# Kernel tuning notes

Measured on AMD Instinct MI355X. Metric: run time of the kernel, lower is better.

Reference implementation:

```python
import jax, jax.numpy as jnp
import numpy as np

M_CH = 2        # channels == sources
K = 8           # NMF bases
N_ITER = 8
SWITCH_ITER = 5
ALPHA = 0.1
BETA = 0.0
EPS = 1e-10
I_BINS = 1025   # freq bins (n_fft=2048)
J_FRAMES = 4096 # STFT frames


def setup_inputs() -> dict:
    key = jax.random.key(0)
    ks = jax.random.split(key, 5)
    X = jax.random.normal(ks[0], (M_CH, J_FRAMES, I_BINS, 2), jnp.float32)
    T_s = jax.random.uniform(ks[1], (I_BINS, K), jnp.float32) * 0.1 + EPS
    V_s = jax.random.uniform(ks[2], (K, J_FRAMES), jnp.float32) * 0.1 + EPS
    T_n = jax.random.uniform(ks[3], (I_BINS, K), jnp.float32) * 0.1 + EPS
    V_n = jax.random.uniform(ks[4], (K, J_FRAMES), jnp.float32) * 0.1 + EPS
    return {"X": X, "T_s": T_s, "V_s": V_s, "T_n": T_n, "V_n": V_n}


def _ilrma_noisy(X, T_s, V_s, T_n, V_n):
    M, J, I, _ = X.shape
    eps, alpha, beta = EPS, ALPHA, BETA
    # (M,J,I,2) -> complex (I,M,J)
    Xc = (X[..., 0] + 1j * X[..., 1]).astype(jnp.complex64).transpose(2, 0, 1)
    eyeM = jnp.eye(M, dtype=jnp.complex64)
    W = jnp.broadcast_to(eyeM, (I, M, M))
    Y = jnp.einsum('inm,inj->imj', W.conj(), Xc)  # W^H X
    lam_n = jnp.ones((I,), jnp.float32)
    r_s = jnp.maximum(T_s @ V_s, eps)
    r_n = jnp.maximum(T_n @ V_n, eps)

    for it in range(N_ITER):
        if it < SWITCH_ITER:
            r_s = jnp.maximum(T_s @ V_s, eps)
            r_n = jnp.maximum(T_n @ V_n, eps)
        lam = lam_n[:, None]
        Lam = jnp.maximum(r_s + r_n * lam, eps)
        Y1 = Y[:, 0, :]
        p1 = jnp.abs(Y1) ** 2                          # (I,J)
        pn = jnp.sum(jnp.abs(Y[:, 1:, :]) ** 2, axis=1)  # (I,J)
        invL = 1.0 / Lam
        invL2 = invL * invL
        if it < SWITCH_ITER:
            # --- T_s ---
            T_s = jnp.maximum(T_s * jnp.sqrt(((p1 * invL2) @ V_s.T) / ((invL @ V_s.T) + eps)), eps)
            r_s = jnp.maximum(T_s @ V_s, eps)
            Lam = jnp.maximum(r_s + r_n * lam, eps); invL = 1.0 / Lam; invL2 = invL * invL
            # --- V_s ---
            V_s = jnp.maximum(V_s * jnp.sqrt((T_s.T @ (p1 * invL2)) / ((T_s.T @ invL) + eps)), eps)
            r_s = jnp.maximum(T_s @ V_s, eps)
            Lam = jnp.maximum(r_s + r_n * lam, eps); invL = 1.0 / Lam; invL2 = invL * invL
            inv_rn = 1.0 / r_n; inv_rn2 = inv_rn * inv_rn
            # --- T_n ---
            Tn_num = (lam * p1 * invL2) @ V_n.T + (pn * inv_rn2) @ V_n.T
            Tn_den = (lam * invL) @ V_n.T + (M - 1) * (inv_rn @ V_n.T) + eps
            T_n = jnp.maximum(T_n * jnp.sqrt(Tn_num / Tn_den), eps)
            r_n = jnp.maximum(T_n @ V_n, eps)
            Lam = jnp.maximum(r_s + r_n * lam, eps); invL = 1.0 / Lam; invL2 = invL * invL
            inv_rn = 1.0 / r_n; inv_rn2 = inv_rn * inv_rn
            # --- V_n ---
            Vn_num = T_n.T @ (lam * p1 * invL2) + T_n.T @ (pn * inv_rn2)
            Vn_den = T_n.T @ (lam * invL) + (M - 1) * (T_n.T @ inv_rn) + eps
            V_n = jnp.maximum(V_n * jnp.sqrt(Vn_num / Vn_den), eps)
            r_n = jnp.maximum(T_n @ V_n, eps)
            r_s = jnp.maximum(T_s @ V_s, eps)
            Lam = jnp.maximum(r_s + r_n * lam, eps); invL = 1.0 / Lam; invL2 = invL * invL
            # --- lambda_n ---
            lam_num = jnp.sum(r_n * p1 * invL2, axis=1)
            lam_den = jnp.sum(r_n * invL, axis=1) + eps
            lam_n = jnp.maximum(lam_n * jnp.sqrt(lam_num / lam_den), eps)
            Lam = jnp.maximum(r_s + r_n * lam_n[:, None], eps)
            # --- GEVD demixing update per frequency bin ---
            Xw_s = Xc * jnp.sqrt(1.0 / Lam)[:, None, :]
            Xw_n = Xc * jnp.sqrt(1.0 / r_n)[:, None, :]
            G_s = jnp.einsum('imj,inj->imn', Xw_s, Xw_s.conj()) / J + eps * eyeM
            G_n = jnp.einsum('imj,inj->imn', Xw_n, Xw_n.conj()) / J + eps * eyeM
            L = jnp.linalg.cholesky(G_s)
            Linv = jnp.linalg.inv(L)
            LinvH = jnp.conj(jnp.swapaxes(Linv, 1, 2))
            C = Linv @ G_n @ LinvH
            evals, evecs = jnp.linalg.eigh(C)  # ascending eigenvalues
            Vg = LinvH @ evecs                 # (I,M,M) generalized eigenvectors
            cols = []
            for m in range(M):
                h = Vg[:, :, m]                # (I,M); eigh already sorts ascending
                G = G_s if m == 0 else G_n
                quad = jnp.real(jnp.einsum('im,imn,in->i', h.conj(), G, h))
                cols.append(h / jnp.sqrt(jnp.maximum(quad, eps))[:, None])
            W = jnp.stack(cols, axis=2)
            Y = jnp.einsum('inm,inj->imj', W.conj(), Xc)
        else:
            # Phase 2: fix W, unconstrained r updates with inverse-gamma prior
            inv_rs = 1.0 / (r_s + eps); inv_rs2 = inv_rs * inv_rs
            inv_rn = 1.0 / (r_n + eps); inv_rn2 = inv_rn * inv_rn
            r_s = jnp.maximum(r_s * jnp.sqrt((p1 * invL2 + beta * inv_rs2) / (invL + (alpha + 1.0) * inv_rs + eps)), eps)
            Lam = jnp.maximum(r_s + r_n * lam, eps); invL = 1.0 / Lam; invL2 = invL * invL
            r_n = jnp.maximum(r_n * jnp.sqrt((lam * p1 * invL2 + pn * inv_rn2) / (lam * invL + (M - 1) * inv_rn + eps)), eps)
            Lam = jnp.maximum(r_s + r_n * lam, eps); invL = 1.0 / Lam; invL2 = invL * invL
            lam_num = jnp.sum(r_n * p1 * invL2, axis=1)
            lam_den = jnp.sum(r_n * invL, axis=1) + eps
            lam_n = jnp.maximum(lam_n * jnp.sqrt(lam_num / lam_den), eps)

    # Final single-channel Wiener extraction of the target, replicated over M
    Lam = jnp.maximum(r_s + r_n * lam_n[:, None], eps)
    S = (r_s / Lam) * Y[:, 0, :]                       # (I,J) complex
    S_ri = jnp.stack([jnp.real(S).T, jnp.imag(S).T], axis=-1)  # (J,I,2)
    return jnp.broadcast_to(S_ri[None], (M, J, I, 2)).astype(jnp.float32)


def reference(X, T_s, V_s, T_n, V_n):
    return _ilrma_noisy(X, T_s, V_s, T_n, V_n)
```

## Files before the change

### kernel.cpp

```cpp
#include <hip/hip_runtime.h>
#include <math.h>

#define IB 1025
#define JF 4096
#define EPSF 1e-10f
#define NCH 128

__device__ __forceinline__ void load8(const float* __restrict__ base, int i, float v[8]) {
  const float4* b4 = (const float4*)(base + i * 8);
  float4 a = b4[0], b = b4[1];
  v[0]=a.x; v[1]=a.y; v[2]=a.z; v[3]=a.w; v[4]=b.x; v[5]=b.y; v[6]=b.z; v[7]=b.w;
}
__device__ __forceinline__ float dot8(const float a[8], const float b[8]) {
  float s = a[0]*b[0];
#pragma unroll
  for (int k=1;k<8;k++) s += a[k]*b[k];
  return s;
}
__device__ __forceinline__ float dot8s(const float a[8], const float* __restrict__ b) {
  float s = a[0]*b[0];
#pragma unroll
  for (int k=1;k<8;k++) s += a[k]*b[k];
  return s;
}

#define STAGE_V32(vsh, vnh, Vs, Vn, j0) do {                                \
    int t_ = threadIdx.x;                                                   \
    int jj_ = t_ >> 3, k_ = t_ & 7;                                         \
    vsh[jj_][k_] = Vs[k_*JF + (j0) + jj_];                                  \
    vnh[jj_][k_] = Vn[k_*JF + (j0) + jj_];                                  \
    __syncthreads();                                                        \
  } while (0)

__global__ __launch_bounds__(256) void k_init(
    const float* __restrict__ Ts_in, const float* __restrict__ Vs_in,
    const float* __restrict__ Tn_in, const float* __restrict__ Vn_in,
    float* __restrict__ Ts, float* __restrict__ Vs,
    float* __restrict__ Tn, float* __restrict__ Vn,
    float* __restrict__ lam, float* __restrict__ Wm) {
  int idx = blockIdx.x * 256 + threadIdx.x;
  if (idx < 8 * JF) { Vs[idx] = Vs_in[idx]; Vn[idx] = Vn_in[idx]; }
  if (idx < IB * 8) { Ts[idx] = Ts_in[idx]; Tn[idx] = Tn_in[idx]; }
  if (idx < IB) {
    lam[idx] = 1.0f;
    float* w = Wm + idx * 8;
    w[0]=1.f; w[1]=0.f; w[2]=0.f; w[3]=0.f; w[4]=0.f; w[5]=0.f; w[6]=1.f; w[7]=0.f;
  }
}

__global__ __launch_bounds__(256) void k_p1pn_ts(const float2* __restrict__ X2,
    const float* __restrict__ Wm,
    const float* __restrict__ Ts, const float* __restrict__ Vs,
    const float* __restrict__ Tn, const float* __restrict__ Vn,
    const float* __restrict__ lam,
    float* __restrict__ p1, float* __restrict__ pn, float* __restrict__ P) {
  __shared__ float vsh[32][8], vnh[32][8];
  int tx = threadIdx.x;
  int i = blockIdx.x * 256 + tx;
  int jc = blockIdx.y;
  int j0 = jc * 32;
  STAGE_V32(vsh, vnh, Vs, Vn, j0);
  if (i >= IB) return;
  float ts[8], tn[8];
  load8(Ts, i, ts); load8(Tn, i, tn);
  float lamv = lam[i];
  const float4* W4 = (const float4*)Wm;
  float4 wa = W4[i*2], wb = W4[i*2+1];
  float num[8] = {0,0,0,0,0,0,0,0}, den[8] = {0,0,0,0,0,0,0,0};
#pragma unroll 4
  for (int jj = 0; jj < 32; jj++) {
    int j = j0 + jj;
    float2 x0 = X2[j*IB + i];
    float2 x1 = X2[(JF + j)*IB + i];
    float y0r = wa.x*x0.x + wa.y*x0.y + wa.z*x1.x + wa.w*x1.y;
    float y0i = wa.x*x0.y - wa.y*x0.x + wa.z*x1.y - wa.w*x1.x;
    float y1r = wb.x*x0.x + wb.y*x0.y + wb.z*x1.x + wb.w*x1.y;
    float y1i = wb.x*x0.y - wb.y*x0.x + wb.z*x1.y - wb.w*x1.x;
    float pv  = y0r*y0r + y0i*y0i;
    float pnv = y1r*y1r + y1i*y1i;
    p1[j*IB + i] = pv;
    pn[j*IB + i] = pnv;
    float rs = fmaxf(dot8s(ts, vsh[jj]), EPSF);
    float rn = fmaxf(dot8s(tn, vnh[jj]), EPSF);
    float iL = 1.f / fmaxf(rs + rn*lamv, EPSF);
    float a2 = pv*iL*iL;
#pragma unroll
    for (int k=0;k<8;k++){ num[k] += a2*vsh[jj][k]; den[k] += iL*vsh[jj][k]; }
  }
#pragma unroll
  for (int k=0;k<8;k++){
    P[(jc*16+k)*IB + i] = num[k];
    P[(jc*16+8+k)*IB + i] = den[k];
  }
}

__global__ __launch_bounds__(512) void k_t_final(const float* __restrict__ P, float* __restrict__ T) {
  int tx = threadIdx.x;
  int ii = tx & 63, g = tx >> 6;
  int i = blockIdx.x * 64 + ii;
  int k = blockIdx.y;
  float num = 0.f, den = 0.f;
  if (i < IB) {
    for (int t = 0; t < NCH/8; t++) {
      int c = g*(NCH/8) + t;
      num += P[(c*16+k)*IB + i];
      den += P[(c*16+8+k)*IB + i];
    }
  }
  __shared__ float red[2][8][64];
  red[0][g][ii] = num; red[1][g][ii] = den;
  __syncthreads();
  if (g == 0 && i < IB) {
    float n_ = 0.f, d_ = 0.f;
#pragma unroll
    for (int q=0;q<8;q++){ n_ += red[0][q][ii]; d_ += red[1][q][ii]; }
    float t = T[i*8+k];
    T[i*8+k] = fmaxf(t * sqrtf(n_/(d_+EPSF)), EPSF);
  }
}

__global__ __launch_bounds__(256) void k_vs(const float* __restrict__ p1,
    const float* __restrict__ Ts, float* __restrict__ Vs,
    const float* __restrict__ Tn, const float* __restrict__ Vn,
    const float* __restrict__ lam) {
  int j = blockIdx.x;
  int tx = threadIdx.x;
  float vs[8], vn[8];
#pragma unroll
  for (int k=0;k<8;k++){ vs[k]=Vs[k*JF+j]; vn[k]=Vn[k*JF+j]; }
  float acc[16];
#pragma unroll
  for (int v=0;v<16;v++) acc[v] = 0.f;
  for (int s = 0; s < 5; s++) {
    int i = s*256 + tx;
    if (i < IB) {
      float ts[8], tn[8];
      load8(Ts, i, ts); load8(Tn, i, tn);
      float lamv = lam[i];
      float pv = p1[j*IB + i];
      float rs = fmaxf(dot8(ts, vs), EPSF);
      float rn = fmaxf(dot8(tn, vn), EPSF);
      float iL = 1.f / fmaxf(rs + rn*lamv, EPSF);
      float a2 = pv*iL*iL;
#pragma unroll
      for (int k=0;k<8;k++){ acc[k] += ts[k]*a2; acc[8+k] += ts[k]*iL; }
    }
  }
  __shared__ float red[4][16];
  int wid = tx >> 6, lane = tx & 63;
#pragma unroll
  for (int v=0;v<16;v++){
    float x = acc[v];
    x += __shfl_down(x, 32, 64); x += __shfl_down(x, 16, 64);
    x += __shfl_down(x, 8, 64);  x += __shfl_down(x, 4, 64);
    x += __shfl_down(x, 2, 64);  x += __shfl_down(x, 1, 64);
    if (lane == 0) red[wid][v] = x;
  }
  __syncthreads();
  if (tx == 0) {
#pragma unroll
    for (int k=0;k<8;k++){
      float n_ = red[0][k]+red[1][k]+red[2][k]+red[3][k];
      float d_ = red[0][8+k]+red[1][8+k]+red[2][8+k]+red[3][8+k];
      Vs[k*JF+j] = fmaxf(vs[k] * sqrtf(n_/(d_+EPSF)), EPSF);
    }
  }
}

__global__ __launch_bounds__(256) void k_tn_partial(const float* __restrict__ p1,
    const float* __restrict__ pn,
    const float* __restrict__ Ts, const float* __restrict__ Vs,
    const float* __restrict__ Tn, const float* __restrict__ Vn,
    const float* __restrict__ lam, float* __restrict__ P) {
  __shared__ float vsh[32][8], vnh[32][8];
  int tx = threadIdx.x;
  int i = blockIdx.x * 256 + tx;
  int jc = blockIdx.y;
  int j0 = jc * 32;
  STAGE_V32(vsh, vnh, Vs, Vn, j0);
  if (i >= IB) return;
  float ts[8], tn[8];
  load8(Ts, i, ts); load8(Tn, i, tn);
  float lamv = lam[i];
  float num[8] = {0,0,0,0,0,0,0,0}, den[8] = {0,0,0,0,0,0,0,0};
#pragma unroll 4
  for (int jj = 0; jj < 32; jj++) {
    int j = j0 + jj;
    float pv = p1[j*IB + i];
    float pnv = pn[j*IB + i];
    float rs = fmaxf(dot8s(ts, vsh[jj]), EPSF);
    float rn = fmaxf(dot8s(tn, vnh[jj]), EPSF);
    float iL = 1.f / fmaxf(rs + rn*lamv, EPSF);
    float irn = 1.f / rn;
    float a2 = lamv*pv*iL*iL + pnv*irn*irn;
    float b2 = lamv*iL + irn;
#pragma unroll
    for (int k=0;k<8;k++){ num[k] += a2*vnh[jj][k]; den[k] += b2*vnh[jj][k]; }
  }
#pragma unroll
  for (int k=0;k<8;k++){
    P[(jc*16+k)*IB + i] = num[k];
    P[(jc*16+8+k)*IB + i] = den[k];
  }
}

__global__ __launch_bounds__(256) void k_vn(const float* __restrict__ p1,
    const float* __restrict__ pn,
    const float* __restrict__ Ts, const float* __restrict__ Vs,
    const float* __restrict__ Tn, float* __restrict__ Vn,
    const float* __restrict__ lam) {
  int j = blockIdx.x;
  int tx = threadIdx.x;
  float vs[8], vn[8];
#pragma unroll
  for (int k=0;k<8;k++){ vs[k]=Vs[k*JF+j]; vn[k]=Vn[k*JF+j]; }
  float acc[16];
#pragma unroll
  for (int v=0;v<16;v++) acc[v] = 0.f;
  for (int s = 0; s < 5; s++) {
    int i = s*256 + tx;
    if (i < IB) {
      float ts[8], tn[8];
      load8(Ts, i, ts); load8(Tn, i, tn);
      float lamv = lam[i];
      float pv = p1[j*IB + i];
      float pnv = pn[j*IB + i];
      float rs = fmaxf(dot8(ts, vs), EPSF);
      float rn = fmaxf(dot8(tn, vn), EPSF);
      float iL = 1.f / fmaxf(rs + rn*lamv, EPSF);
      float irn = 1.f / rn;
      float a2 = lamv*pv*iL*iL + pnv*irn*irn;
      float b2 = lamv*iL + irn;
#pragma unroll
      for (int k=0;k<8;k++){ acc[k] += tn[k]*a2; acc[8+k] += tn[k]*b2; }
    }
  }
  __shared__ float red[4][16];
  int wid = tx >> 6, lane = tx & 63;
#pragma unroll
  for (int v=0;v<16;v++){
    float x = acc[v];
    x += __shfl_down(x, 32, 64); x += __shfl_down(x, 16, 64);
    x += __shfl_down(x, 8, 64);  x += __shfl_down(x, 4, 64);
    x += __shfl_down(x, 2, 64);  x += __shfl_down(x, 1, 64);
    if (lane == 0) red[wid][v] = x;
  }
  __syncthreads();
  if (tx == 0) {
#pragma unroll
    for (int k=0;k<8;k++){
      float n_ = red[0][k]+red[1][k]+red[2][k]+red[3][k];
      float d_ = red[0][8+k]+red[1][8+k]+red[2][8+k]+red[3][8+k];
      Vn[k*JF+j] = fmaxf(vn[k] * sqrtf(n_/(d_+EPSF)), EPSF);
    }
  }
}

__global__ __launch_bounds__(256) void k_lam_partial(const float* __restrict__ p1,
    const float* __restrict__ Ts, const float* __restrict__ Vs,
    const float* __restrict__ Tn, const float* __restrict__ Vn,
    const float* __restrict__ lam, float* __restrict__ P) {
  __shared__ float vsh[32][8], vnh[32][8];
  int tx = threadIdx.x;
  int i = blockIdx.x * 256 + tx;
  int jc = blockIdx.y;
  int j0 = jc * 32;
  STAGE_V32(vsh, vnh, Vs, Vn, j0);
  if (i >= IB) return;
  float ts[8], tn[8];
  load8(Ts, i, ts); load8(Tn, i, tn);
  float lamv = lam[i];
  float lnum = 0.f, lden = 0.f;
#pragma unroll 4
  for (int jj = 0; jj < 32; jj++) {
    int j = j0 + jj;
    float pv = p1[j*IB + i];
    float rs = fmaxf(dot8s(ts, vsh[jj]), EPSF);
    float rn = fmaxf(dot8s(tn, vnh[jj]), EPSF);
    float iL = 1.f / fmaxf(rs + rn*lamv, EPSF);
    lnum += rn*pv*iL*iL;
    lden += rn*iL;
  }
  P[(jc*2+0)*IB + i] = lnum;
  P[(jc*2+1)*IB + i] = lden;
}

__global__ __launch_bounds__(512) void k_lam_final(const float* __restrict__ P, float* __restrict__ lam,
                                                   int nchunks) {
  int tx = threadIdx.x;
  int ii = tx & 63, g = tx >> 6;
  int i = blockIdx.x * 64 + ii;
  int per = nchunks >> 3;
  float num = 0.f, den = 0.f;
  if (i < IB) {
    for (int t = 0; t < per; t++) {
      int c = g*per + t;
      num += P[(c*2+0)*IB + i];
      den += P[(c*2+1)*IB + i];
    }
  }
  __shared__ float red[2][8][64];
  red[0][g][ii] = num; red[1][g][ii] = den;
  __syncthreads();
  if (g == 0 && i < IB) {
    float n_ = 0.f, d_ = 0.f;
#pragma unroll
    for (int q=0;q<8;q++){ n_ += red[0][q][ii]; d_ += red[1][q][ii]; }
    lam[i] = fmaxf(lam[i] * sqrtf(n_/(d_+EPSF)), EPSF);
  }
}

__global__ __launch_bounds__(256) void k_g_partial(const float2* __restrict__ X2,
    const float* __restrict__ Ts, const float* __restrict__ Vs,
    const float* __restrict__ Tn, const float* __restrict__ Vn,
    const float* __restrict__ lam, float* __restrict__ P) {
  __shared__ float vsh[32][8], vnh[32][8];
  int tx = threadIdx.x;
  int i = blockIdx.x * 256 + tx;
  int jc = blockIdx.y;
  int j0 = jc * 32;
  STAGE_V32(vsh, vnh, Vs, Vn, j0);
  if (i >= IB) return;
  float ts[8], tn[8];
  load8(Ts, i, ts); load8(Tn, i, tn);
  float lamv = lam[i];
  float g[8];
#pragma unroll
  for (int v=0;v<8;v++) g[v] = 0.f;
#pragma unroll 4
  for (int jj = 0; jj < 32; jj++) {
    int j = j0 + jj;
    float2 x0 = X2[j*IB + i];
    float2 x1 = X2[(JF + j)*IB + i];
    float rs = fmaxf(dot8s(ts, vsh[jj]), EPSF);
    float rn = fmaxf(dot8s(tn, vnh[jj]), EPSF);
    float ws = 1.f / fmaxf(rs + rn*lamv, EPSF);
    float wn = 1.f / rn;
    float m00 = x0.x*x0.x + x0.y*x0.y;
    float m11 = x1.x*x1.x + x1.y*x1.y;
    float m01r = x0.x*x1.x + x0.y*x1.y;
    float m01i = x0.y*x1.x - x0.x*x1.y;
    g[0] += m00*ws; g[1] += m11*ws; g[2] += m01r*ws; g[3] += m01i*ws;
    g[4] += m00*wn; g[5] += m11*wn; g[6] += m01r*wn; g[7] += m01i*wn;
  }
#pragma unroll
  for (int v=0;v<8;v++) P[(jc*8+v)*IB + i] = g[v];
}

__device__ void dlaev2_dev(double a, double b, double c,
                           double& rt1, double& rt2, double& cs1, double& sn1) {
  double sm = a + c, df = a - c;
  double adf = fabs(df);
  double tb = b + b;
  double ab = fabs(tb);
  double acmx, acmn;
  if (fabs(a) > fabs(c)) { acmx = a; acmn = c; } else { acmx = c; acmn = a; }
  double rt;
  if (adf > ab)      { double t = ab/adf; rt = adf*sqrt(1.0 + t*t); }
  else if (adf < ab) { double t = adf/ab; rt = ab*sqrt(1.0 + t*t); }
  else               rt = ab*sqrt(2.0);
  int sgn1;
  if (sm < 0.0)      { rt1 = 0.5*(sm - rt); sgn1 = -1; rt2 = (acmx/rt1)*acmn - (b/rt1)*b; }
  else if (sm > 0.0) { rt1 = 0.5*(sm + rt); sgn1 =  1; rt2 = (acmx/rt1)*acmn - (b/rt1)*b; }
  else               { rt1 = 0.5*rt; rt2 = -0.5*rt; sgn1 = 1; }
  double cs; int sgn2;
  if (df >= 0.0) { cs = df + rt; sgn2 = 1; } else { cs = df - rt; sgn2 = -1; }
  double acs = fabs(cs);
  if (acs > ab) {
    double ct = -tb/cs;
    sn1 = 1.0/sqrt(1.0 + ct*ct);
    cs1 = ct*sn1;
  } else {
    if (ab == 0.0) { cs1 = 1.0; sn1 = 0.0; }
    else { double tn = -cs/tb; cs1 = 1.0/sqrt(1.0 + tn*tn); sn1 = tn*cs1; }
  }
  if (sgn1 == sgn2) { double tn = cs1; cs1 = -sn1; sn1 = tn; }
}

__global__ __launch_bounds__(512) void k_geig(const float* __restrict__ P, float* __restrict__ Wm) {
  int tx = threadIdx.x;
  int ii = tx & 63, v = tx >> 6;
  int i = blockIdx.x * 64 + ii;
  double s = 0.0;
  if (i < IB) {
    for (int c = 0; c < NCH; c++) s += (double)P[(c*8+v)*IB + i];
  }
  __shared__ double gsh[8][64];
  gsh[v][ii] = s;
  __syncthreads();
  if (v != 0 || i >= IB) return;
  const double EPSD = 1e-10;
  double as  = gsh[0][ii]/4096.0 + EPSD;
  double cs_ = gsh[1][ii]/4096.0 + EPSD;
  double bsr = gsh[2][ii]/4096.0, bsi = gsh[3][ii]/4096.0;
  double dn  = gsh[4][ii]/4096.0 + EPSD;
  double fn  = gsh[5][ii]/4096.0 + EPSD;
  double enr = gsh[6][ii]/4096.0, eni = gsh[7][ii]/4096.0;
  double l11 = sqrt(as);
  double il11 = 1.0/l11;
  double l21r = bsr*il11, l21i = -bsi*il11;
  double l22sq = cs_ - (l21r*l21r + l21i*l21i);
  double l22 = sqrt(fmax(l22sq, 0.0));
  double p = il11, r = 1.0/l22;
  double qr = -l21r*p*r, qi = -l21i*p*r;
  double C00  = p*p*dn;
  double C01r = p*(dn*qr + enr*r);
  double C01i = p*(-dn*qi + eni*r);
  double C11  = (qr*qr+qi*qi)*dn + 2.0*r*(qr*enr - qi*eni) + r*r*fn;
  double br = C01r, bi = C01i;
  double e_, hqr, hqi;
  if (bi == 0.0) { e_ = br; hqr = 1.0; hqi = 0.0; }
  else {
    double ab_ = sqrt(br*br + bi*bi);
    e_ = (br >= 0.0) ? -ab_ : ab_;
    hqr = br / e_; hqi = -bi / e_;
  }
  double ut0, ub0, ut1, ub1;
  const double MEPS = 1.1102230246251565e-16;
  if (fabs(e_) <= sqrt(fabs(C00))*sqrt(fabs(C11))*MEPS) {
    if (C11 < C00) { ut0=0.0; ub0=1.0; ut1=1.0; ub1=0.0; }
    else           { ut0=1.0; ub0=0.0; ut1=0.0; ub1=1.0; }
  } else {
    double rt1, rt2, cs1, sn1;
    dlaev2_dev(C00, e_, C11, rt1, rt2, cs1, sn1);
    if (rt2 < rt1) { ut0=-sn1; ub0=cs1; ut1=cs1;  ub1=sn1; }
    else           { ut0=cs1;  ub0=sn1; ut1=-sn1; ub1=cs1; }
  }
  double chr = qr*hqr + qi*hqi;
  double chi = qr*hqi - qi*hqr;
  double v0tr = p*ut0 + chr*ub0, v0ti = chi*ub0;
  double v0br = r*hqr*ub0,       v0bi = r*hqi*ub0;
  double v1tr = p*ut1 + chr*ub1, v1ti = chi*ub1;
  double v1br = r*hqr*ub1,       v1bi = r*hqi*ub1;
  double q0 = as*(v0tr*v0tr+v0ti*v0ti) + cs_*(v0br*v0br+v0bi*v0bi)
            + 2.0*((bsr*v0br - bsi*v0bi)*v0tr + (bsr*v0bi + bsi*v0br)*v0ti);
  double q1 = dn*(v1tr*v1tr+v1ti*v1ti) + fn*(v1br*v1br+v1bi*v1bi)
            + 2.0*((enr*v1br - eni*v1bi)*v1tr + (enr*v1bi + eni*v1br)*v1ti);
  double s0 = 1.0/sqrt(fmax(q0, 1e-10));
  double s1 = 1.0/sqrt(fmax(q1, 1e-10));
  float* w = Wm + i*8;
  w[0] = (float)(v0tr*s0); w[1] = (float)(v0ti*s0);
  w[2] = (float)(v0br*s0); w[3] = (float)(v0bi*s0);
  w[4] = (float)(v1tr*s1); w[5] = (float)(v1ti*s1);
  w[6] = (float)(v1br*s1); w[7] = (float)(v1bi*s1);
}

__global__ __launch_bounds__(256) void k_p1pn_rinit(const float2* __restrict__ X2,
    const float* __restrict__ Wm,
    const float* __restrict__ Ts, const float* __restrict__ Vs,
    const float* __restrict__ Tn, const float* __restrict__ Vn,
    float* __restrict__ p1, float* __restrict__ pn, float2* __restrict__ m0) {
  int i = blockIdx.x * 256 + threadIdx.x;
  int j = blockIdx.y;
  if (i >= IB) return;
  float2 x0 = X2[j*IB + i];
  float2 x1 = X2[(JF + j)*IB + i];
  const float4* W4 = (const float4*)Wm;
  float4 wa = W4[i*2], wb = W4[i*2+1];
  float y0r = wa.x*x0.x + wa.y*x0.y + wa.z*x1.x + wa.w*x1.y;
  float y0i = wa.x*x0.y - wa.y*x0.x + wa.z*x1.y - wa.w*x1.x;
  float y1r = wb.x*x0.x + wb.y*x0.y + wb.z*x1.x + wb.w*x1.y;
  float y1i = wb.x*x0.y - wb.y*x0.x + wb.z*x1.y - wb.w*x1.x;
  p1[j*IB + i] = y0r*y0r + y0i*y0i;
  pn[j*IB + i] = y1r*y1r + y1i*y1i;
  float ts[8], tn[8];
  load8(Ts, i, ts); load8(Tn, i, tn);
  float rs = 0.f, rn = 0.f;
#pragma unroll
  for (int k=0;k<8;k++){ rs += ts[k]*Vs[k*JF+j]; rn += tn[k]*Vn[k*JF+j]; }
  m0[j*IB + i] = make_float2(fmaxf(rs, EPSF), fmaxf(rn, EPSF));
}

__global__ __launch_bounds__(256) void k_simp(float2* __restrict__ m0,
    const float* __restrict__ p1, const float* __restrict__ pn,
    const float* __restrict__ lam, float* __restrict__ P) {
  int tx = threadIdx.x;
  int i = blockIdx.x * 256 + tx;
  int jc = blockIdx.y;
  if (i >= IB) return;
  float lamv = lam[i];
  float lnum = 0.f, lden = 0.f;
  int j0 = jc * 32;
#pragma unroll 4
  for (int jj = 0; jj < 32; jj++) {
    int j = j0 + jj;
    float2 rr = m0[j*IB + i];
    float rs = rr.x, rn = rr.y;
    float pv = p1[j*IB + i], pnv = pn[j*IB + i];
    float iL = 1.f / fmaxf(rs + rn*lamv, EPSF);
    float irs = 1.f / (rs + EPSF);
    float rs2 = fmaxf(rs * sqrtf((pv*iL*iL) / (iL + 1.1f*irs + EPSF)), EPSF);
    float iL2 = 1.f / fmaxf(rs2 + rn*lamv, EPSF);
    float irn = 1.f / (rn + EPSF);
    float rn2 = fmaxf(rn * sqrtf((lamv*pv*iL2*iL2 + pnv*irn*irn) / (lamv*iL2 + irn + EPSF)), EPSF);
    float iL3 = 1.f / fmaxf(rs2 + rn2*lamv, EPSF);
    m0[j*IB + i] = make_float2(rs2, rn2);
    lnum += rn2*pv*iL3*iL3;
    lden += rn2*iL3;
  }
  P[(jc*2+0)*IB + i] = lnum;
  P[(jc*2+1)*IB + i] = lden;
}

__global__ __launch_bounds__(256) void k_final(float2* __restrict__ m0, float2* __restrict__ m1,
    const float2* __restrict__ X2, const float* __restrict__ Wm, const float* __restrict__ lam) {
  int i = blockIdx.x * 256 + threadIdx.x;
  int j = blockIdx.y;
  if (i >= IB) return;
  float2 rr = m0[j*IB + i];
  float L = fmaxf(rr.x + rr.y*lam[i], EPSF);
  float gsc = rr.x / L;
  float2 x0 = X2[j*IB + i];
  float2 x1 = X2[(JF + j)*IB + i];
  float4 wa = ((const float4*)Wm)[i*2];
  float y0r = wa.x*x0.x + wa.y*x0.y + wa.z*x1.x + wa.w*x1.y;
  float y0i = wa.x*x0.y - wa.y*x0.x + wa.z*x1.y - wa.w*x1.x;
  float2 s = make_float2(gsc*y0r, gsc*y0i);
  m0[j*IB + i] = s;
  m1[j*IB + i] = s;
}

extern "C" void kernel_launch(void* const* d_in, const int* in_sizes, int n_in,
                              void* d_out, int out_size, void* d_ws, size_t ws_size,
                              hipStream_t stream) {
  (void)in_sizes; (void)n_in; (void)out_size; (void)ws_size;
  const float* X = (const float*)d_in[0];
  const float* Ts_in = (const float*)d_in[1];
  const float* Vs_in = (const float*)d_in[2];
  const float* Tn_in = (const float*)d_in[3];
  const float* Vn_in = (const float*)d_in[4];

  float* w = (float*)d_ws;
  float* Pt  = w;
  float* Ts  = w + 1049600 + 16448;
  float* Vs  = Ts + 8200;
  float* Tn  = Vs + 32768;
  float* Vn  = Tn + 8200;
  float* lam = Vn + 32768;
  float* Wm  = lam + 1028;

  float* out = (float*)d_out;
  float2* m0 = (float2*)d_out;
  float2* m1 = m0 + (size_t)JF*IB;
  float* p1 = out + 2*(size_t)JF*IB;
  float* pn = p1 + (size_t)JF*IB;
  float* Pbig = out;
  const float2* X2 = (const float2*)X;

  k_init<<<dim3(128), 256, 0, stream>>>(Ts_in, Vs_in, Tn_in, Vn_in, Ts, Vs, Tn, Vn, lam, Wm);

  for (int it = 0; it < 5; it++) {
    k_p1pn_ts<<<dim3(5, NCH), 256, 0, stream>>>(X2, Wm, Ts, Vs, Tn, Vn, lam, p1, pn, Pbig);
    k_t_final<<<dim3(17, 8), 512, 0, stream>>>(Pbig, Ts);
    k_vs<<<dim3(JF), 256, 0, stream>>>(p1, Ts, Vs, Tn, Vn, lam);
    k_tn_partial<<<dim3(5, NCH), 256, 0, stream>>>(p1, pn, Ts, Vs, Tn, Vn, lam, Pbig);
    k_t_final<<<dim3(17, 8), 512, 0, stream>>>(Pbig, Tn);
    k_vn<<<dim3(JF), 256, 0, stream>>>(p1, pn, Ts, Vs, Tn, Vn, lam);
    k_lam_partial<<<dim3(5, NCH), 256, 0, stream>>>(p1, Ts, Vs, Tn, Vn, lam, Pbig);
    k_lam_final<<<dim3(17), 512, 0, stream>>>(Pbig, lam, NCH);
    k_g_partial<<<dim3(5, NCH), 256, 0, stream>>>(X2, Ts, Vs, Tn, Vn, lam, Pbig);
    k_geig<<<dim3(17), 512, 0, stream>>>(Pbig, Wm);
  }

  k_p1pn_rinit<<<dim3(5, JF), 256, 0, stream>>>(X2, Wm, Ts, Vs, Tn, Vn, p1, pn, m0);

  for (int it = 0; it < 3; it++) {
    k_simp<<<dim3(5, NCH), 256, 0, stream>>>(m0, p1, pn, lam, Pt);
    k_lam_final<<<dim3(17), 512, 0, stream>>>(Pt, lam, NCH);
  }

  k_final<<<dim3(5, JF), 256, 0, stream>>>(m0, m1, X2, Wm, lam);
}
```

Before: 894.4 us.

## Halve j-chunk size to 16 and fuse r-init with first simplified iteration

Doubles the number of j-chunks (NCH 128→256, 16 frames per block) in all partial-reduction kernels to raise block count and occupancy, with V staging split across thread halves. It also fuses the post-switch p1/pn/r initialisation kernel with the first simplified r_s/r_n/lambda update, removing one full pass that writes m0 and then rereads it along with p1 and pn. The trade-off is more partial sums for the final reducers to combine and more per-block setup overhead.

```diff
diff --git a/kernel.cpp b/kernel.cpp
--- a/kernel.cpp
+++ b/kernel.cpp
@@ -4,7 +4,7 @@
 #define IB 1025
 #define JF 4096
 #define EPSF 1e-10f
-#define NCH 128
+#define NCH 256
 
 __device__ __forceinline__ void load8(const float* __restrict__ base, int i, float v[8]) {
   const float4* b4 = (const float4*)(base + i * 8);
@@ -24,11 +24,12 @@
   return s;
 }
 
-#define STAGE_V32(vsh, vnh, Vs, Vn, j0) do {                                \
+#define STAGE_V16(vsh, vnh, Vs, Vn, j0) do {                                \
     int t_ = threadIdx.x;                                                   \
-    int jj_ = t_ >> 3, k_ = t_ & 7;                                         \
-    vsh[jj_][k_] = Vs[k_*JF + (j0) + jj_];                                  \
-    vnh[jj_][k_] = Vn[k_*JF + (j0) + jj_];                                  \
+    if (t_ < 128) { int jj_ = t_ >> 3, k_ = t_ & 7;                         \
+      vsh[jj_][k_] = Vs[k_*JF + (j0) + jj_]; }                              \
+    else { int u_ = t_ - 128; int jj_ = u_ >> 3, k_ = u_ & 7;               \
+      vnh[jj_][k_] = Vn[k_*JF + (j0) + jj_]; }                              \
     __syncthreads();                                                        \
   } while (0)
 
@@ -54,12 +55,12 @@
     const float* __restrict__ Tn, const float* __restrict__ Vn,
     const float* __restrict__ lam,
     float* __restrict__ p1, float* __restrict__ pn, float* __restrict__ P) {
-  __shared__ float vsh[32][8], vnh[32][8];
+  __shared__ float vsh[16][8], vnh[16][8];
   int tx = threadIdx.x;
   int i = blockIdx.x * 256 + tx;
   int jc = blockIdx.y;
-  int j0 = jc * 32;
-  STAGE_V32(vsh, vnh, Vs, Vn, j0);
+  int j0 = jc * 16;
+  STAGE_V16(vsh, vnh, Vs, Vn, j0);
   if (i >= IB) return;
   float ts[8], tn[8];
   load8(Ts, i, ts); load8(Tn, i, tn);
@@ -67,8 +68,8 @@
   const float4* W4 = (const float4*)Wm;
   float4 wa = W4[i*2], wb = W4[i*2+1];
   float num[8] = {0,0,0,0,0,0,0,0}, den[8] = {0,0,0,0,0,0,0,0};
-#pragma unroll 4
-  for (int jj = 0; jj < 32; jj++) {
+#pragma unroll 8
+  for (int jj = 0; jj < 16; jj++) {
     int j = j0 + jj;
     float2 x0 = X2[j*IB + i];
     float2 x1 = X2[(JF + j)*IB + i];
@@ -172,19 +173,19 @@
     const float* __restrict__ Ts, const float* __restrict__ Vs,
     const float* __restrict__ Tn, const float* __restrict__ Vn,
     const float* __restrict__ lam, float* __restrict__ P) {
-  __shared__ float vsh[32][8], vnh[32][8];
+  __shared__ float vsh[16][8], vnh[16][8];
   int tx = threadIdx.x;
   int i = blockIdx.x * 256 + tx;
   int jc = blockIdx.y;
-  int j0 = jc * 32;
-  STAGE_V32(vsh, vnh, Vs, Vn, j0);
+  int j0 = jc * 16;
+  STAGE_V16(vsh, vnh, Vs, Vn, j0);
   if (i >= IB) return;
   float ts[8], tn[8];
   load8(Ts, i, ts); load8(Tn, i, tn);
   float lamv = lam[i];
   float num[8] = {0,0,0,0,0,0,0,0}, den[8] = {0,0,0,0,0,0,0,0};
-#pragma unroll 4
-  for (int jj = 0; jj < 32; jj++) {
+#pragma unroll 8
+  for (int jj = 0; jj < 16; jj++) {
     int j = j0 + jj;
     float pv = p1[j*IB + i];
     float pnv = pn[j*IB + i];
@@ -260,19 +261,19 @@
     const float* __restrict__ Ts, const float* __restrict__ Vs,
     const float* __restrict__ Tn, const float* __restrict__ Vn,
     const float* __restrict__ lam, float* __restrict__ P) {
-  __shared__ float vsh[32][8], vnh[32][8];
+  __shared__ float vsh[16][8], vnh[16][8];
   int tx = threadIdx.x;
   int i = blockIdx.x * 256 + tx;
   int jc = blockIdx.y;
-  int j0 = jc * 32;
-  STAGE_V32(vsh, vnh, Vs, Vn, j0);
+  int j0 = jc * 16;
+  STAGE_V16(vsh, vnh, Vs, Vn, j0);
   if (i >= IB) return;
   float ts[8], tn[8];
   load8(Ts, i, ts); load8(Tn, i, tn);
   float lamv = lam[i];
   float lnum = 0.f, lden = 0.f;
-#pragma unroll 4
-  for (int jj = 0; jj < 32; jj++) {
+#pragma unroll 8
+  for (int jj = 0; jj < 16; jj++) {
     int j = j0 + jj;
     float pv = p1[j*IB + i];
     float rs = fmaxf(dot8s(ts, vsh[jj]), EPSF);
@@ -314,12 +315,12 @@
     const float* __restrict__ Ts, const float* __restrict__ Vs,
     const float* __restrict__ Tn, const float* __restrict__ Vn,
     const float* __restrict__ lam, float* __restrict__ P) {
-  __shared__ float vsh[32][8], vnh[32][8];
+  __shared__ float vsh[16][8], vnh[16][8];
   int tx = threadIdx.x;
   int i = blockIdx.x * 256 + tx;
   int jc = blockIdx.y;
-  int j0 = jc * 32;
-  STAGE_V32(vsh, vnh, Vs, Vn, j0);
+  int j0 = jc * 16;
+  STAGE_V16(vsh, vnh, Vs, Vn, j0);
   if (i >= IB) return;
   float ts[8], tn[8];
   load8(Ts, i, ts); load8(Tn, i, tn);
@@ -327,8 +328,8 @@
   float g[8];
 #pragma unroll
   for (int v=0;v<8;v++) g[v] = 0.f;
-#pragma unroll 4
-  for (int jj = 0; jj < 32; jj++) {
+#pragma unroll 8
+  for (int jj = 0; jj < 16; jj++) {
     int j = j0 + jj;
     float2 x0 = X2[j*IB + i];
     float2 x1 = X2[(JF + j)*IB + i];
@@ -445,30 +446,54 @@
   w[6] = (float)(v1br*s1); w[7] = (float)(v1bi*s1);
 }
 
-__global__ __launch_bounds__(256) void k_p1pn_rinit(const float2* __restrict__ X2,
+__global__ __launch_bounds__(256) void k_rinit_simp(const float2* __restrict__ X2,
     const float* __restrict__ Wm,
     const float* __restrict__ Ts, const float* __restrict__ Vs,
     const float* __restrict__ Tn, const float* __restrict__ Vn,
-    float* __restrict__ p1, float* __restrict__ pn, float2* __restrict__ m0) {
-  int i = blockIdx.x * 256 + threadIdx.x;
-  int j = blockIdx.y;
-  if (i >= IB) return;
-  float2 x0 = X2[j*IB + i];
-  float2 x1 = X2[(JF + j)*IB + i];
+    const float* __restrict__ lam,
+    float* __restrict__ p1, float* __restrict__ pn, float2* __restrict__ m0,
+    float* __restrict__ P) {
+  __shared__ float vsh[16][8], vnh[16][8];
+  int tx = threadIdx.x;
+  int i = blockIdx.x * 256 + tx;
+  int jc = blockIdx.y;
+  int j0 = jc * 16;
+  STAGE_V16(vsh, vnh, Vs, Vn, j0);
+  if (i >= IB) return;
+  float ts[8], tn[8];
+  load8(Ts, i, ts); load8(Tn, i, tn);
+  float lamv = lam[i];
   const float4* W4 = (const float4*)Wm;
   float4 wa = W4[i*2], wb = W4[i*2+1];
-  float y0r = wa.x*x0.x + wa.y*x0.y + wa.z*x1.x + wa.w*x1.y;
-  float y0i = wa.x*x0.y - wa.y*x0.x + wa.z*x1.y - wa.w*x1.x;
-  float y1r = wb.x*x0.x + wb.y*x0.y + wb.z*x1.x + wb.w*x1.y;
-  float y1i = wb.x*x0.y - wb.y*x0.x + wb.z*x1.y - wb.w*x1.x;
-  p1[j*IB + i] = y0r*y0r + y0i*y0i;
-  pn[j*IB + i] = y1r*y1r + y1i*y1i;
-  float ts[8], tn[8];
-  load8(Ts, i, ts); load8(Tn, i, tn);
-  float rs = 0.f, rn = 0.f;
-#pragma unroll
-  for (int k=0;k<8;k++){ rs += ts[k]*Vs[k*JF+j]; rn += tn[k]*Vn[k*JF+j]; }
-  m0[j*IB + i] = make_float2(fmaxf(rs, EPSF), fmaxf(rn, EPSF));
+  float lnum = 0.f, lden = 0.f;
+#pragma unroll 8
+  for (int jj = 0; jj < 16; jj++) {
+    int j = j0 + jj;
+    float2 x0 = X2[j*IB + i];
+    float2 x1 = X2[(JF + j)*IB + i];
+    float y0r = wa.x*x0.x + wa.y*x0.y + wa.z*x1.x + wa.w*x1.y;
+    float y0i = wa.x*x0.y - wa.y*x0.x + wa.z*x1.y - wa.w*x1.x;
+    float y1r = wb.x*x0.x + wb.y*x0.y + wb.z*x1.x + wb.w*x1.y;
+    float y1i = wb.x*x0.y - wb.y*x0.x + wb.z*x1.y - wb.w*x1.x;
+    float pv  = y0r*y0r + y0i*y0i;
+    float pnv = y1r*y1r + y1i*y1i;
+    p1[j*IB + i] = pv;
+    pn[j*IB + i] = pnv;
+    float rs = fmaxf(dot8s(ts, vsh[jj]), EPSF);
+    float rn = fmaxf(dot8s(tn, vnh[jj]), EPSF);
+    float iL = 1.f / fmaxf(rs + rn*lamv, EPSF);
+    float irs = 1.f / (rs + EPSF);
+    float rs2 = fmaxf(rs * sqrtf((pv*iL*iL) / (iL + 1.1f*irs + EPSF)), EPSF);
+    float iL2 = 1.f / fmaxf(rs2 + rn*lamv, EPSF);
+    float irn = 1.f / (rn + EPSF);
+    float rn2 = fmaxf(rn * sqrtf((lamv*pv*iL2*iL2 + pnv*irn*irn) / (lamv*iL2 + irn + EPSF)), EPSF);
+    float iL3 = 1.f / fmaxf(rs2 + rn2*lamv, EPSF);
+    m0[j*IB + i] = make_float2(rs2, rn2);
+    lnum += rn2*pv*iL3*iL3;
+    lden += rn2*iL3;
+  }
+  P[(jc*2+0)*IB + i] = lnum;
+  P[(jc*2+1)*IB + i] = lden;
 }
 
 __global__ __launch_bounds__(256) void k_simp(float2* __restrict__ m0,
@@ -480,9 +505,9 @@
   if (i >= IB) return;
   float lamv = lam[i];
   float lnum = 0.f, lden = 0.f;
-  int j0 = jc * 32;
-#pragma unroll 4
-  for (int jj = 0; jj < 32; jj++) {
+  int j0 = jc * 16;
+#pragma unroll 8
+  for (int jj = 0; jj < 16; jj++) {
     int j = j0 + jj;
     float2 rr = m0[j*IB + i];
     float rs = rr.x, rn = rr.y;
@@ -562,9 +587,10 @@
     k_geig<<<dim3(17), 512, 0, stream>>>(Pbig, Wm);
   }
 
-  k_p1pn_rinit<<<dim3(5, JF), 256, 0, stream>>>(X2, Wm, Ts, Vs, Tn, Vn, p1, pn, m0);
-
-  for (int it = 0; it < 3; it++) {
+  k_rinit_simp<<<dim3(5, NCH), 256, 0, stream>>>(X2, Wm, Ts, Vs, Tn, Vn, lam, p1, pn, m0, Pt);
+  k_lam_final<<<dim3(17), 512, 0, stream>>>(Pt, lam, NCH);
+
+  for (int it = 0; it < 2; it++) {
     k_simp<<<dim3(5, NCH), 256, 0, stream>>>(m0, p1, pn, lam, Pt);
     k_lam_final<<<dim3(17), 512, 0, stream>>>(Pt, lam, NCH);
   }
```

After: 922.6 us. 3.1% more time.
